# Performance work log

Measured on AMD Instinct MI355X. Metric: run time of the kernel, lower is better.

The kernel has to match this reference:

```python
import jax, jax.numpy as jnp
import numpy as np

B, T, K = 128, 4096, 64
START, STOP = 62, 63
NEG = -10000.0


def setup_inputs() -> dict:
    key = jax.random.key(0)
    k1, k2, k3 = jax.random.split(key, 3)
    feats = jax.random.normal(k1, (B, T, K), dtype=jnp.float32)
    # gold tags never include START/STOP
    tags = jax.random.randint(k2, (B, T), 0, START)
    transitions = jax.random.normal(k3, (K, K), dtype=jnp.float32)
    # mirror the torch __init__ masking: no transition INTO start, none OUT of stop
    transitions = transitions.at[START, :].set(NEG).at[:, STOP].set(NEG)
    return {"feats": feats, "tags": tags, "transitions": transitions}


def _crf_single(feats, tags, transitions):
    """feats: [T,K], tags: [T], transitions: [K,K] (trans[next, prev])."""
    init = jnp.full((K,), NEG, dtype=feats.dtype).at[START].set(0.0)

    # ---- forward algorithm (log partition), vectorized over the tag loop ----
    def fwd_step(alpha, feat):
        # alpha[i] + trans[j, i] + feat[j]  ->  logsumexp over prev i
        new = jax.nn.logsumexp(alpha[None, :] + transitions, axis=1) + feat
        return new, None

    alpha, _ = jax.lax.scan(fwd_step, init, feats)
    forward_score = jax.nn.logsumexp(alpha + transitions[STOP])

    # ---- gold path score (_score_session) ----
    prev_tags = jnp.concatenate([jnp.array([START], dtype=tags.dtype), tags[:-1]])
    emit = jnp.take_along_axis(feats, tags[:, None], axis=1)[:, 0]  # feats[t, tags[t]]
    gold_score = jnp.sum(transitions[tags, prev_tags] + emit) + transitions[STOP, tags[-1]]

    nll = forward_score - gold_score  # neg_log_likelihood

    # ---- Viterbi decode ----
    def vit_step(delta, feat):
        scores = delta[None, :] + transitions  # [next, prev]
        bp = jnp.argmax(scores, axis=1)
        new = jnp.max(scores, axis=1) + feat  # feat added after argmax, as in torch
        return new, bp

    delta, bps = jax.lax.scan(vit_step, init, feats)  # bps: [T, K]
    terminal = delta + transitions[STOP]
    best_last = jnp.argmax(terminal)
    path_score = terminal[best_last]

    def back_step(tag, bp_t):
        return bp_t[tag], tag

    _, best_path = jax.lax.scan(back_step, best_last, bps, reverse=True)  # [T]
    return nll, path_score, best_path


def reference(feats, tags, transitions):
    nll, path_score, best_path = jax.vmap(_crf_single, in_axes=(0, 0, None))(
        feats, tags, transitions
    )
    return nll, path_score, best_path
```

## Files before the change

kernel.cpp:

```cpp
#include <hip/hip_runtime.h>

namespace {
constexpr int Tn = 4096;
constexpr int Kn = 64;
constexpr int BATCH = 128;
constexpr int START_TAG = 62;
constexpr int STOP_TAG = 63;
constexpr float NEGV = -10000.0f;
constexpr int CH = 64;
constexpr int NCH = Tn / CH;
constexpr int GL = 8;
constexpr int NG = Tn / GL;
constexpr int WV = 4;
constexpr int SL = Kn / WV;
constexpr int KP = 66;

__device__ __forceinline__ float rfl(float x) {
    return __uint_as_float(__builtin_amdgcn_readfirstlane(__float_as_uint(x)));
}
__device__ __forceinline__ void bar() {
    __asm__ volatile("s_waitcnt lgkmcnt(0)\n\ts_barrier" ::: "memory");
}
__device__ __forceinline__ void vmdrain() {
    __asm__ volatile("s_waitcnt vmcnt(0)" ::: "memory");
}
__device__ __forceinline__ unsigned int fkey(float x) {
    unsigned int b = __float_as_uint(x);
    return (b & 0x80000000u) ? ~b : (b | 0x80000000u);
}
__device__ __forceinline__ float unkey(unsigned int hb) {
    return __uint_as_float((hb & 0x80000000u) ? (hb ^ 0x80000000u) : ~hb);
}

__global__ __launch_bounds__(256)
void crf_kernel(const float* __restrict__ feats,
                const int* __restrict__ tags,
                const float* __restrict__ trans,
                float* __restrict__ out,
                unsigned int* __restrict__ bp32)
{
    const int tid = threadIdx.x;
    const int lane = tid & 63;
    const int wid = tid >> 6;
    const int b = blockIdx.x & (BATCH - 1);
    const size_t fb = (size_t)b * Tn * Kn;

    __shared__ float sb[2][Kn];
    __shared__ unsigned long long kp[2][WV * KP];
    __shared__ float wp[2][WV * KP];
    __shared__ unsigned char snap[NCH * Kn];
    __shared__ unsigned char echain[NCH];

    if (blockIdx.x < BATCH) {
        float gold = 0.0f;
        if (wid == 0) {
            const int t0 = lane * (Tn / 64);
            int prev = (lane == 0) ? START_TAG : tags[(size_t)b * Tn + t0 - 1];
            for (int k = 0; k < Tn / 64; ++k) {
                const int t = t0 + k;
                const int tg = tags[(size_t)b * Tn + t];
                gold += trans[tg * Kn + prev] + feats[fb + (size_t)t * Kn + tg];
                prev = tg;
            }
            if (lane == 63) gold += trans[STOP_TAG * Kn + prev];
            #pragma unroll
            for (int off = 32; off; off >>= 1) gold += __shfl_down(gold, off);
        }
        float ES[SL];
        #pragma unroll
        for (int q = 0; q < SL / 4; ++q) {
            const float4 t4 = ((const float4*)(trans + lane * Kn + wid * SL))[q];
            ES[4*q+0] = __expf(t4.x); ES[4*q+1] = __expf(t4.y);
            ES[4*q+2] = __expf(t4.z); ES[4*q+3] = __expf(t4.w);
        }
        if (wid == 0) sb[0][lane] = (lane == START_TAG) ? 1.0f : 0.0f;
        float O = 0.0f, v = 0.0f;

        float fc[GL], fn[GL], Fc[GL];
        #pragma unroll
        for (int k = 0; k < GL; ++k) fc[k] = feats[fb + (size_t)k * Kn + lane];
        bar();
        for (int g = 0; g < NG; ++g) {
            if (g + 1 < NG) {
                const size_t base = fb + (size_t)(g + 1) * GL * Kn + lane;
                #pragma unroll
                for (int k = 0; k < GL; ++k) fn[k] = feats[base + (size_t)k * Kn];
            }
            #pragma unroll
            for (int k = 0; k < GL; ++k) Fc[k] = __expf(fc[k]);
            #pragma unroll
            for (int k = 0; k < GL; ++k) {
                const int t = g * GL + k;
                const int p = t & 1;
                const float4* vp = (const float4*)&sb[p][wid * SL];
                const float4 v0 = vp[0], v1 = vp[1], v2 = vp[2], v3 = vp[3];
                float s0 = 0.f, s1 = 0.f, s2 = 0.f, s3 = 0.f;
                s0 = fmaf(ES[0],  v0.x, s0); s1 = fmaf(ES[1],  v0.y, s1);
                s2 = fmaf(ES[2],  v0.z, s2); s3 = fmaf(ES[3],  v0.w, s3);
                s0 = fmaf(ES[4],  v1.x, s0); s1 = fmaf(ES[5],  v1.y, s1);
                s2 = fmaf(ES[6],  v1.z, s2); s3 = fmaf(ES[7],  v1.w, s3);
                s0 = fmaf(ES[8],  v2.x, s0); s1 = fmaf(ES[9],  v2.y, s1);
                s2 = fmaf(ES[10], v2.z, s2); s3 = fmaf(ES[11], v2.w, s3);
                s0 = fmaf(ES[12], v3.x, s0); s1 = fmaf(ES[13], v3.y, s1);
                s2 = fmaf(ES[14], v3.z, s2); s3 = fmaf(ES[15], v3.w, s3);
                wp[p][wid * KP + lane] = (s0 + s1) + (s2 + s3);
                bar();
                const float w0r = wp[p][0 * KP + lane];
                const float w1r = wp[p][1 * KP + lane];
                const float w2r = wp[p][2 * KP + lane];
                const float w3r = wp[p][3 * KP + lane];
                const float w = ((w0r + w1r) + (w2r + w3r)) * Fc[k];
                const float wz = rfl(w);
                O += __logf(wz);
                v = w * __builtin_amdgcn_rcpf(wz);
                if (wid == 0) sb[p ^ 1][lane] = v;
                bar();
            }
            #pragma unroll
            for (int k = 0; k < GL; ++k) fc[k] = fn[k];
        }
        if (wid == 0) {
            const float a = O + __logf(v);
            const float x = a + trans[STOP_TAG * Kn + lane];
            float mx = x;
            #pragma unroll
            for (int off = 32; off; off >>= 1) mx = fmaxf(mx, __shfl_xor(mx, off));
            float se = __expf(x - mx);
            #pragma unroll
            for (int off = 32; off; off >>= 1) se += __shfl_xor(se, off);
            if (lane == 0) out[b] = (mx + __logf(se)) - gold;
        }
    } else {
        float trS[SL];
        #pragma unroll
        for (int q = 0; q < SL / 4; ++q) {
            const float4 t4 = ((const float4*)(trans + lane * Kn + wid * SL))[q];
            trS[4*q+0] = t4.x; trS[4*q+1] = t4.y;
            trS[4*q+2] = t4.z; trS[4*q+3] = t4.w;
        }
        if (wid == 0) sb[0][lane] = (lane == START_TAG) ? 0.0f : NEGV;
        float d = 0.0f;
        int h = lane;
        unsigned int bp4 = 0;
        const size_t dwb = (size_t)b * (Tn / 4);

        float fc[GL], fn[GL];
        #pragma unroll
        for (int k = 0; k < GL; ++k) fc[k] = feats[fb + (size_t)k * Kn + lane];
        bar();
        for (int g = 0; g < NG; ++g) {
            if (g + 1 < NG) {
                const size_t base = fb + (size_t)(g + 1) * GL * Kn + lane;
                #pragma unroll
                for (int k = 0; k < GL; ++k) fn[k] = feats[base + (size_t)k * Kn];
            }
            #pragma unroll
            for (int k = 0; k < GL; ++k) {
                const int t = g * GL + k;
                const int p = t & 1;
                const float4* dp = (const float4*)&sb[p][wid * SL];
                float gv[4]; int gi[4];
                #pragma unroll
                for (int q = 0; q < 4; ++q) {
                    const float4 dv = dp[q];
                    const int i0 = wid * SL + 4 * q;
                    const float sx = dv.x + trS[4*q+0];
                    const float sy = dv.y + trS[4*q+1];
                    const float sz = dv.z + trS[4*q+2];
                    const float sw = dv.w + trS[4*q+3];
                    const bool c01 = sy > sx;
                    const float v01 = c01 ? sy : sx; const int i01 = c01 ? i0+1 : i0;
                    const bool c23 = sw > sz;
                    const float v23 = c23 ? sw : sz; const int i23 = c23 ? i0+3 : i0+2;
                    const bool cq = v23 > v01;
                    gv[q] = cq ? v23 : v01; gi[q] = cq ? i23 : i01;
                }
                const bool ca = gv[1] > gv[0];
                const float va = ca ? gv[1] : gv[0]; const int ia = ca ? gi[1] : gi[0];
                const bool cb = gv[3] > gv[2];
                const float vb = cb ? gv[3] : gv[2]; const int ib = cb ? gi[3] : gi[2];
                const bool cm = vb > va;
                const float m = cm ? vb : va; const int li = cm ? ib : ia;
                kp[p][wid * KP + lane] =
                    ((unsigned long long)fkey(m) << 32) | (unsigned long long)(63 - li);
                bar();
                const unsigned long long k0 = kp[p][0 * KP + lane];
                const unsigned long long k1 = kp[p][1 * KP + lane];
                const unsigned long long k2 = kp[p][2 * KP + lane];
                const unsigned long long k3 = kp[p][3 * KP + lane];
                const unsigned long long ka = k0 > k1 ? k0 : k1;
                const unsigned long long kb = k2 > k3 ? k2 : k3;
                const unsigned long long km = ka > kb ? ka : kb;
                const int bp = 63 - (int)(unsigned int)(km & 0xffffffffULL);
                d = unkey((unsigned int)(km >> 32)) + fc[k];
                if (wid == 0) sb[p ^ 1][lane] = d;
                if (wid == 3) {
                    if ((k & 3) == 0) bp4 = (unsigned int)bp;
                    else bp4 |= (unsigned int)bp << (8 * (k & 3));
                    if ((k & 3) == 3)
                        bp32[(dwb + (size_t)(2 * g + (k >> 2))) * Kn + lane] = bp4;
                    h = __shfl(h, bp);
                    if ((t & (CH - 1)) == (CH - 1)) {
                        snap[(t >> 6) * Kn + lane] = (unsigned char)h;
                        h = lane;
                    }
                }
                bar();
            }
            #pragma unroll
            for (int k = 0; k < GL; ++k) fc[k] = fn[k];
        }
        vmdrain();
        if (wid == 3) {
            const float term = d + trans[STOP_TAG * Kn + lane];
            float bv = term;
            int bi = lane;
            #pragma unroll
            for (int off = 32; off; off >>= 1) {
                const float ov = __shfl_xor(bv, off);
                const int oi = __shfl_xor(bi, off);
                if (ov > bv || (ov == bv && oi < bi)) { bv = ov; bi = oi; }
            }
            if (lane == 0) {
                out[BATCH + b] = bv;
                int e = bi;
                for (int c = NCH - 1; c >= 0; --c) {
                    echain[c] = (unsigned char)e;
                    e = snap[c * Kn + e];
                }
            }
        }
        bar();
        if (wid == 0) {
            int tag = echain[lane];
            float* po = out + 2 * BATCH + (size_t)b * Tn;
            for (int k = CH - 1; k >= 0; --k) {
                const int t = lane * CH + k;
                po[t] = (float)tag;
                tag = (int)((bp32[(dwb + (size_t)(t >> 2)) * Kn + tag] >> (8 * (t & 3))) & 63u);
            }
        }
    }
}
}

extern "C" void kernel_launch(void* const* d_in, const int* in_sizes, int n_in,
                              void* d_out, int out_size, void* d_ws, size_t ws_size,
                              hipStream_t stream)
{
    const float* feats = (const float*)d_in[0];
    const int* tags   = (const int*)d_in[1];
    const float* trans = (const float*)d_in[2];
    float* out = (float*)d_out;
    unsigned int* bp = (unsigned int*)d_ws;
    hipLaunchKernelGGL(crf_kernel, dim3(2 * BATCH), dim3(256), 0, stream,
                       feats, tags, trans, out, bp);
}
```

Before: 1.740 ms.

## Give each wave its own state copy to drop one barrier per step

In both the forward and Viterbi recurrences, every wave now writes its own private double-buffered copy of the state vector instead of having wave 0 publish one shared copy. Each wave only reads back what it wrote itself, so the second block barrier in each time step can be removed, leaving one barrier per step in the latency-bound serial loop. The gold-path score is also spread across all four waves and combined through shared memory. The cost is extra LDS space and redundant per-wave stores, and correctness now depends on the single remaining barrier protecting the double-buffered partial-sum arrays.

Result: faster. 1.653 ms (-5.0%).

```diff
diff --git a/kernel.cpp b/kernel.cpp
--- a/kernel.cpp
+++ b/kernel.cpp
@@ -45,26 +45,29 @@
     const int b = blockIdx.x & (BATCH - 1);
     const size_t fb = (size_t)b * Tn * Kn;
 
-    __shared__ float sb[2][Kn];
+    __shared__ float pvs[WV][2][Kn];
+    __shared__ float wp[2][WV * KP];
+    __shared__ float dvs[WV][2][Kn];
     __shared__ unsigned long long kp[2][WV * KP];
-    __shared__ float wp[2][WV * KP];
+    __shared__ float gw[WV];
     __shared__ unsigned char snap[NCH * Kn];
     __shared__ unsigned char echain[NCH];
 
     if (blockIdx.x < BATCH) {
         float gold = 0.0f;
-        if (wid == 0) {
-            const int t0 = lane * (Tn / 64);
-            int prev = (lane == 0) ? START_TAG : tags[(size_t)b * Tn + t0 - 1];
-            for (int k = 0; k < Tn / 64; ++k) {
+        {
+            const int t0 = tid * (Tn / 256);
+            int prev = (tid == 0) ? START_TAG : tags[(size_t)b * Tn + t0 - 1];
+            for (int k = 0; k < Tn / 256; ++k) {
                 const int t = t0 + k;
                 const int tg = tags[(size_t)b * Tn + t];
                 gold += trans[tg * Kn + prev] + feats[fb + (size_t)t * Kn + tg];
                 prev = tg;
             }
-            if (lane == 63) gold += trans[STOP_TAG * Kn + prev];
+            if (tid == 255) gold += trans[STOP_TAG * Kn + prev];
             #pragma unroll
             for (int off = 32; off; off >>= 1) gold += __shfl_down(gold, off);
+            if (lane == 0) gw[wid] = gold;
         }
         float ES[SL];
         #pragma unroll
@@ -73,7 +76,7 @@
             ES[4*q+0] = __expf(t4.x); ES[4*q+1] = __expf(t4.y);
             ES[4*q+2] = __expf(t4.z); ES[4*q+3] = __expf(t4.w);
         }
-        if (wid == 0) sb[0][lane] = (lane == START_TAG) ? 1.0f : 0.0f;
+        pvs[wid][0][lane] = (lane == START_TAG) ? 1.0f : 0.0f;
         float O = 0.0f, v = 0.0f;
 
         float fc[GL], fn[GL], Fc[GL];
@@ -92,7 +95,7 @@
             for (int k = 0; k < GL; ++k) {
                 const int t = g * GL + k;
                 const int p = t & 1;
-                const float4* vp = (const float4*)&sb[p][wid * SL];
+                const float4* vp = (const float4*)&pvs[wid][p][wid * SL];
                 const float4 v0 = vp[0], v1 = vp[1], v2 = vp[2], v3 = vp[3];
                 float s0 = 0.f, s1 = 0.f, s2 = 0.f, s3 = 0.f;
                 s0 = fmaf(ES[0],  v0.x, s0); s1 = fmaf(ES[1],  v0.y, s1);
@@ -113,8 +116,7 @@
                 const float wz = rfl(w);
                 O += __logf(wz);
                 v = w * __builtin_amdgcn_rcpf(wz);
-                if (wid == 0) sb[p ^ 1][lane] = v;
-                bar();
+                pvs[wid][p ^ 1][lane] = v;
             }
             #pragma unroll
             for (int k = 0; k < GL; ++k) fc[k] = fn[k];
@@ -128,7 +130,8 @@
             float se = __expf(x - mx);
             #pragma unroll
             for (int off = 32; off; off >>= 1) se += __shfl_xor(se, off);
-            if (lane == 0) out[b] = (mx + __logf(se)) - gold;
+            if (lane == 0)
+                out[b] = (mx + __logf(se)) - (((gw[0] + gw[1]) + (gw[2] + gw[3])));
         }
     } else {
         float trS[SL];
@@ -138,7 +141,7 @@
             trS[4*q+0] = t4.x; trS[4*q+1] = t4.y;
             trS[4*q+2] = t4.z; trS[4*q+3] = t4.w;
         }
-        if (wid == 0) sb[0][lane] = (lane == START_TAG) ? 0.0f : NEGV;
+        dvs[wid][0][lane] = (lane == START_TAG) ? 0.0f : NEGV;
         float d = 0.0f;
         int h = lane;
         unsigned int bp4 = 0;
@@ -158,7 +161,7 @@
             for (int k = 0; k < GL; ++k) {
                 const int t = g * GL + k;
                 const int p = t & 1;
-                const float4* dp = (const float4*)&sb[p][wid * SL];
+                const float4* dp = (const float4*)&dvs[wid][p][wid * SL];
                 float gv[4]; int gi[4];
                 #pragma unroll
                 for (int q = 0; q < 4; ++q) {
@@ -193,7 +196,7 @@
                 const unsigned long long km = ka > kb ? ka : kb;
                 const int bp = 63 - (int)(unsigned int)(km & 0xffffffffULL);
                 d = unkey((unsigned int)(km >> 32)) + fc[k];
-                if (wid == 0) sb[p ^ 1][lane] = d;
+                dvs[wid][p ^ 1][lane] = d;
                 if (wid == 3) {
                     if ((k & 3) == 0) bp4 = (unsigned int)bp;
                     else bp4 |= (unsigned int)bp << (8 * (k & 3));
@@ -205,7 +208,6 @@
                         h = lane;
                     }
                 }
-                bar();
             }
             #pragma unroll
             for (int k = 0; k < GL; ++k) fc[k] = fn[k];
```
